# Kernel tuning notes

Measured on AMD Instinct MI355X. Metric: run time of the kernel, lower is better.

## Reference

```python
import jax, jax.numpy as jnp
import numpy as np

N_NODES = 100000
N_EDGES = 1_600_000
F_IN, HID, N_CLS = 128, 64, 32
NEG_SLOPE = 0.2  # PyG GATv2Conv default


def _segment_softmax(scores, seg, num_segments):
    # numerically stable softmax over edges grouped by destination node
    m = jax.ops.segment_max(scores, seg, num_segments=num_segments)
    ex = jnp.exp(scores - m[seg])
    s = jax.ops.segment_sum(ex, seg, num_segments=num_segments)
    return ex / (s[seg] + 1e-16)


def _gatv2_layer(x, src, dst, Wl, bl, Wr, br, att, bias, num_nodes):
    xl = x @ Wl + bl              # source transform  [N, C]
    xr = x @ Wr + br              # target transform  [N, C]
    # per-edge GATv2 attention logit: a . leaky_relu(xl_j + xr_i)
    e = jax.nn.leaky_relu(xl[src] + xr[dst], NEG_SLOPE) @ att  # [E]
    alpha = _segment_softmax(e, dst, num_nodes)                 # [E]
    out = jax.ops.segment_sum(alpha[:, None] * xl[src], dst, num_segments=num_nodes)
    return out + bias


def _add_self_loops(edge_index, n):
    loops = jnp.arange(n, dtype=edge_index.dtype)
    return jnp.concatenate([edge_index, jnp.stack([loops, loops])], axis=1)


def setup_inputs() -> dict:
    key = jax.random.key(0)
    ks = jax.random.split(key, 8)
    s1 = 1.0 / np.sqrt(F_IN)
    s2 = 1.0 / np.sqrt(HID)
    return {
        "x": jax.random.normal(ks[0], (N_NODES, F_IN), jnp.float32),
        "edge_index": jax.random.randint(ks[1], (2, N_EDGES), 0, N_NODES, jnp.int64),
        "W1l": jax.random.normal(ks[2], (F_IN, HID), jnp.float32) * s1,
        "b1l": jnp.zeros((HID,), jnp.float32),
        "W1r": jax.random.normal(ks[3], (F_IN, HID), jnp.float32) * s1,
        "b1r": jnp.zeros((HID,), jnp.float32),
        "att1": jax.random.normal(ks[4], (HID,), jnp.float32) * s2,
        "bias1": jnp.zeros((HID,), jnp.float32),
        "W2l": jax.random.normal(ks[5], (HID, N_CLS), jnp.float32) * s2,
        "b2l": jnp.zeros((N_CLS,), jnp.float32),
        "W2r": jax.random.normal(ks[6], (HID, N_CLS), jnp.float32) * s2,
        "b2r": jnp.zeros((N_CLS,), jnp.float32),
        "att2": jax.random.normal(ks[7], (N_CLS,), jnp.float32) / np.sqrt(N_CLS),
        "bias2": jnp.zeros((N_CLS,), jnp.float32),
    }


def reference(x, edge_index, W1l, b1l, W1r, b1r, att1, bias1,
              W2l, b2l, W2r, b2r, att2, bias2):
    n = x.shape[0]
    ei = _add_self_loops(edge_index, n)
    src, dst = ei[0], ei[1]
    h = jax.nn.relu(_gatv2_layer(x, src, dst, W1l, b1l, W1r, b1r, att1, bias1, n))
    # F.dropout(training=False) is identity in eval mode
    out = _gatv2_layer(h, src, dst, W2l, b2l, W2r, b2r, att2, bias2, n)
    return out
```

## Files before the change

kernel.cpp:

```cpp
#include <hip/hip_runtime.h>
#include <math.h>

#define F_IN 128
#define HID 64
#define NCLS 32
#define NEG 0.2f
#define NBKT 256
#define CHUNK 8192

using bf8 = __attribute__((ext_vector_type(8))) short;
using f4v = __attribute__((ext_vector_type(4))) float;

__device__ __forceinline__ void f4fma(float4& a, float s, const float4& w) {
    a.x = fmaf(s, w.x, a.x);
    a.y = fmaf(s, w.y, a.y);
    a.z = fmaf(s, w.z, a.z);
    a.w = fmaf(s, w.w, a.w);
}
__device__ __forceinline__ unsigned short f2bf(float f) {
    unsigned u = __float_as_uint(f);
    return (unsigned short)((u + 0x7FFFu + ((u >> 16) & 1u)) >> 16);
}


__global__ __launch_bounds__(256) void zeroBuckets(int* __restrict__ bucketSize, int BK) {
    int i = blockIdx.x * 256 + threadIdx.x;
    if (i < BK) bucketSize[i] = 0;
}

__global__ __launch_bounds__(256) void bucketHist(const int* __restrict__ ei,
                                                  int Eorig, int Etot,
                                                  int* __restrict__ bucketSize, int BK) {
    __shared__ int h[512];
    int t = threadIdx.x;
    for (int j = t; j < BK; j += 256) h[j] = 0;
    __syncthreads();
    int base = blockIdx.x * CHUNK;
    int end = base + CHUNK < Etot ? base + CHUNK : Etot;
    for (int i = base + t; i < end; i += 256) {
        int dst = i < Eorig ? ei[Eorig + i] : i - Eorig;
        atomicAdd(&h[dst >> 8], 1);
    }
    __syncthreads();
    for (int j = t; j < BK; j += 256)
        if (h[j]) atomicAdd(&bucketSize[j], h[j]);
}

__global__ __launch_bounds__(256) void bucketScan(const int* __restrict__ bucketSize,
                                                  int* __restrict__ bucketStart,
                                                  int* __restrict__ bucketCursor,
                                                  int BK, int Etot) {
    __shared__ int sd[256];
    int t = threadIdx.x;
    int v0 = (2 * t     < BK) ? bucketSize[2 * t]     : 0;
    int v1 = (2 * t + 1 < BK) ? bucketSize[2 * t + 1] : 0;
    int ts = v0 + v1;
    sd[t] = ts;
    __syncthreads();
    for (int off = 1; off < 256; off <<= 1) {
        int x = (t >= off) ? sd[t - off] : 0;
        __syncthreads();
        sd[t] += x;
        __syncthreads();
    }
    int excl = sd[t] - ts;
    if (2 * t < BK)     { bucketStart[2 * t] = excl;          bucketCursor[2 * t] = excl; }
    if (2 * t + 1 < BK) { bucketStart[2 * t + 1] = excl + v0; bucketCursor[2 * t + 1] = excl + v0; }
    if (t == 255) bucketStart[BK] = Etot;
}

__global__ __launch_bounds__(256) void bucketScatter(const int* __restrict__ ei,
                                                     int Eorig, int Etot,
                                                     int* __restrict__ bucketCursor,
                                                     int2* __restrict__ pairs, int BK) {
    __shared__ int h[512], lbase[512], hcur[512];
    int t = threadIdx.x;
    for (int j = t; j < BK; j += 256) { h[j] = 0; hcur[j] = 0; }
    __syncthreads();
    int base = blockIdx.x * CHUNK;
    int end = base + CHUNK < Etot ? base + CHUNK : Etot;
    for (int i = base + t; i < end; i += 256) {
        int dst = i < Eorig ? ei[Eorig + i] : i - Eorig;
        atomicAdd(&h[dst >> 8], 1);
    }
    __syncthreads();
    for (int j = t; j < BK; j += 256)
        lbase[j] = h[j] ? atomicAdd(&bucketCursor[j], h[j]) : 0;
    __syncthreads();
    for (int i = base + t; i < end; i += 256) {
        int src, dst;
        if (i < Eorig) { src = ei[i]; dst = ei[Eorig + i]; }
        else           { src = dst = i - Eorig; }
        int b = dst >> 8;
        int off = atomicAdd(&hcur[b], 1);
        pairs[lbase[b] + off] = make_int2(src, dst);
    }
}

__global__ __launch_bounds__(256) void bucketCSR(const int2* __restrict__ pairs,
                                                 const int* __restrict__ bucketStart,
                                                 int* __restrict__ rowstart,
                                                 int* __restrict__ cnt,
                                                 int* __restrict__ srclist, int N) {
    __shared__ int c[256], cur[256];
    int t = threadIdx.x;
    int b = blockIdx.x;
    int lo = b * NBKT;
    int eb = bucketStart[b], ee = bucketStart[b + 1];
    c[t] = 0;
    __syncthreads();
    for (int i = eb + t; i < ee; i += 256)
        atomicAdd(&c[pairs[i].y - lo], 1);
    __syncthreads();
    cur[t] = c[t];
    __syncthreads();
    for (int off = 1; off < 256; off <<= 1) {
        int x = (t >= off) ? cur[t - off] : 0;
        __syncthreads();
        cur[t] += x;
        __syncthreads();
    }
    int excl = cur[t] - c[t];
    int node = lo + t;
    if (node < N) { rowstart[node] = eb + excl; cnt[node] = c[t]; }
    __syncthreads();
    cur[t] = excl;
    __syncthreads();
    for (int i = eb + t; i < ee; i += 256) {
        int2 pr = pairs[i];
        int pos = atomicAdd(&cur[pr.y - lo], 1);
        srclist[eb + pos] = pr.x;
    }
}

__global__ __launch_bounds__(256) void prepW(const float* __restrict__ Wl,
                                             const float* __restrict__ Wr,
                                             uint4* __restrict__ wfrag) {
    int e = blockIdx.x * 256 + threadIdx.x;
    if (e >= 2048) return;
    int lane = e & 63;
    int kt = (e >> 6) & 3;
    int ct = (e >> 8) & 3;
    int mat = e >> 10;
    const float* W = mat ? Wr : Wl;
    int k0 = kt * 32 + (lane >> 4) * 8;
    int c = ct * 16 + (lane & 15);
    unsigned short h[8];
#pragma unroll
    for (int j = 0; j < 8; j++) h[j] = f2bf(W[(k0 + j) * HID + c]);
    wfrag[e] = *(uint4*)h;
}

__global__ __launch_bounds__(256) void transform1(const float* __restrict__ x,
                                                  const uint4* __restrict__ wfrag,
                                                  const float* __restrict__ bl,
                                                  const float* __restrict__ br,
                                                  unsigned short* __restrict__ xlb,
                                                  float* __restrict__ xr, int N) {
    __shared__ uint4 sw[2048];
    int t = threadIdx.x;
#pragma unroll
    for (int j = 0; j < 8; j++) sw[t + j * 256] = wfrag[t + j * 256];
    __syncthreads();

    int w = t >> 6, lane = t & 63;
    int nb = blockIdx.x * 64 + w * 16;
    int m = lane & 15, quad = lane >> 4;

    int arow = nb + m; if (arow >= N) arow = N - 1;
    const float* xrow = x + (size_t)arow * F_IN + quad * 8;
    bf8 afr[4];
#pragma unroll
    for (int kt = 0; kt < 4; kt++) {
        float4 lo = *(const float4*)(xrow + kt * 32);
        float4 hi = *(const float4*)(xrow + kt * 32 + 4);
        unsigned short hh[8];
        hh[0] = f2bf(lo.x); hh[1] = f2bf(lo.y); hh[2] = f2bf(lo.z); hh[3] = f2bf(lo.w);
        hh[4] = f2bf(hi.x); hh[5] = f2bf(hi.y); hh[6] = f2bf(hi.z); hh[7] = f2bf(hi.w);
        afr[kt] = *(bf8*)hh;
    }

#pragma unroll
    for (int mat = 0; mat < 2; mat++) {
        const float* bias = mat ? br : bl;
#pragma unroll
        for (int ct = 0; ct < 4; ct++) {
            f4v acc = {0.f, 0.f, 0.f, 0.f};
#pragma unroll
            for (int kt = 0; kt < 4; kt++) {
                bf8 bfr = *(bf8*)&sw[((mat * 4 + ct) * 4 + kt) * 64 + lane];
                acc = __builtin_amdgcn_mfma_f32_16x16x32_bf16(afr[kt], bfr, acc, 0, 0, 0);
            }
            int ch = ct * 16 + m;
            float bv = bias[ch];
#pragma unroll
            for (int reg = 0; reg < 4; reg++) {
                int node = nb + quad * 4 + reg;
                if (node < N) {
                    float o = acc[reg] + bv;
                    if (mat) xr[(size_t)node * HID + ch] = o;
                    else     xlb[(size_t)node * HID + ch] = f2bf(o);
                }
            }
        }
    }
}

__global__ __launch_bounds__(256) void transform2(const float* __restrict__ h,
                                                  const float* __restrict__ Wl,
                                                  const float* __restrict__ bl,
                                                  const float* __restrict__ Wr,
                                                  const float* __restrict__ br,
                                                  unsigned short* __restrict__ xlb,
                                                  float* __restrict__ xr, int N) {
    __shared__ float sWl[HID * NCLS];
    __shared__ float sWr[HID * NCLS];
    __shared__ float sx[128][68];
    int t = threadIdx.x;
    int nb = blockIdx.x * 128;

#pragma unroll
    for (int j = 0; j < 2; j++) {
        int f = t + j * 256;
        ((float4*)sWl)[f] = ((const float4*)Wl)[f];
        ((float4*)sWr)[f] = ((const float4*)Wr)[f];
    }
    int maxf = (N - nb) * 16;
#pragma unroll
    for (int j = 0; j < 8; j++) {
        int f = t + j * 256;
        int node = f >> 4, kc = f & 15;
        float4 v = {0.f, 0.f, 0.f, 0.f};
        if (f < maxf) v = ((const float4*)(h + (size_t)nb * HID))[f];
        v.x = fmaxf(v.x, 0.f);
        v.y = fmaxf(v.y, 0.f);
        v.z = fmaxf(v.z, 0.f);
        v.w = fmaxf(v.w, 0.f);
        *(float4*)&sx[node][kc * 4] = v;
    }
    __syncthreads();

    int c4 = (t & 7) * 4;
    int slot = t >> 3;
    float4 bl4 = *(const float4*)(bl + c4);
    float4 br4 = *(const float4*)(br + c4);
    float4 accl[4] = {bl4, bl4, bl4, bl4};
    float4 accr[4] = {br4, br4, br4, br4};

#pragma unroll 4
    for (int k4 = 0; k4 < HID / 4; k4++) {
        int k = k4 * 4;
        float4 wl0 = *(const float4*)&sWl[(k + 0) * NCLS + c4];
        float4 wl1 = *(const float4*)&sWl[(k + 1) * NCLS + c4];
        float4 wl2 = *(const float4*)&sWl[(k + 2) * NCLS + c4];
        float4 wl3 = *(const float4*)&sWl[(k + 3) * NCLS + c4];
        float4 wr0 = *(const float4*)&sWr[(k + 0) * NCLS + c4];
        float4 wr1 = *(const float4*)&sWr[(k + 1) * NCLS + c4];
        float4 wr2 = *(const float4*)&sWr[(k + 2) * NCLS + c4];
        float4 wr3 = *(const float4*)&sWr[(k + 3) * NCLS + c4];
#pragma unroll
        for (int j = 0; j < 4; j++) {
            float4 xv = *(const float4*)&sx[slot + j * 32][k];
            f4fma(accl[j], xv.x, wl0); f4fma(accr[j], xv.x, wr0);
            f4fma(accl[j], xv.y, wl1); f4fma(accr[j], xv.y, wr1);
            f4fma(accl[j], xv.z, wl2); f4fma(accr[j], xv.z, wr2);
            f4fma(accl[j], xv.w, wl3); f4fma(accr[j], xv.w, wr3);
        }
    }
#pragma unroll
    for (int j = 0; j < 4; j++) {
        int g = nb + slot + j * 32;
        if (g < N) {
            ushort4 o;
            o.x = f2bf(accl[j].x); o.y = f2bf(accl[j].y);
            o.z = f2bf(accl[j].z); o.w = f2bf(accl[j].w);
            *(ushort4*)(xlb + (size_t)g * NCLS + c4) = o;
            *(float4*)(xr + (size_t)g * NCLS + c4) = accr[j];
        }
    }
}

template <int C>
__global__ __launch_bounds__(256) void fusedAggB(const unsigned short* __restrict__ xlb,
                                                 const float* __restrict__ xr,
                                                 const float* __restrict__ att,
                                                 const int* __restrict__ rowstart,
                                                 const int* __restrict__ cnt,
                                                 const int* __restrict__ srclist,
                                                 const float* __restrict__ bias,
                                                 float* __restrict__ out, int N) {
    const int LPQ = C / 8;
    const int SLOTS = 64 / LPQ;
    int wid = threadIdx.x >> 6;
    int lane = threadIdx.x & 63;
    int n = blockIdx.x * 4 + wid;
    if (n >= N) return;

    int slot = lane / LPQ;
    int pos = lane % LPQ;
    int c8 = pos * 8;

    float xr8[8], at8[8];
    *(float4*)&xr8[0] = *(const float4*)(xr + (size_t)n * C + c8);
    *(float4*)&xr8[4] = *(const float4*)(xr + (size_t)n * C + c8 + 4);
    *(float4*)&at8[0] = *(const float4*)(att + c8);
    *(float4*)&at8[4] = *(const float4*)(att + c8 + 4);

    int row = rowstart[n];
    int deg = cnt[n];

    float s = 0.f;
    float acc[8] = {0.f, 0.f, 0.f, 0.f, 0.f, 0.f, 0.f, 0.f};

    for (int cb = 0; cb < deg; cb += 64) {
        int len = deg - cb; if (len > 64) len = 64;
        int li = lane < len ? lane : len - 1;
        int srcreg = srclist[row + cb + li];
        int nbatch = (len + SLOTS - 1) / SLOTS;
#pragma unroll 4
        for (int b = 0; b < nbatch; b++) {
            int eidx = b * SLOTS + slot;
            int src = __shfl(srcreg, eidx, 64);
            uint4 q = *(const uint4*)(xlb + (size_t)src * C + c8);
            float v[8];
            v[0] = __uint_as_float(q.x << 16);
            v[1] = __uint_as_float(q.x & 0xffff0000u);
            v[2] = __uint_as_float(q.y << 16);
            v[3] = __uint_as_float(q.y & 0xffff0000u);
            v[4] = __uint_as_float(q.z << 16);
            v[5] = __uint_as_float(q.z & 0xffff0000u);
            v[6] = __uint_as_float(q.w << 16);
            v[7] = __uint_as_float(q.w & 0xffff0000u);
            float p = 0.f;
#pragma unroll
            for (int c = 0; c < 8; c++) {
                float u = v[c] + xr8[c];
                u = fmaxf(u, NEG * u);
                p = fmaf(u, at8[c], p);
            }
#pragma unroll
            for (int o = 1; o < LPQ; o <<= 1) p += __shfl_xor(p, o, 64);
            float w = (eidx < len) ? __expf(p) : 0.f;
            s += w;
#pragma unroll
            for (int c = 0; c < 8; c++) acc[c] = fmaf(w, v[c], acc[c]);
        }
    }
#pragma unroll
    for (int o = LPQ; o < 64; o <<= 1) {
#pragma unroll
        for (int c = 0; c < 8; c++) acc[c] += __shfl_xor(acc[c], o, 64);
        s += __shfl_xor(s, o, 64);
    }
    if (lane < LPQ) {
        float bi8[8];
        *(float4*)&bi8[0] = *(const float4*)(bias + c8);
        *(float4*)&bi8[4] = *(const float4*)(bias + c8 + 4);
        float inv = 1.f / (s + 1e-16f);
        float o8[8];
#pragma unroll
        for (int c = 0; c < 8; c++) o8[c] = acc[c] * inv + bi8[c];
        *(float4*)(out + (size_t)n * C + c8)     = *(float4*)&o8[0];
        *(float4*)(out + (size_t)n * C + c8 + 4) = *(float4*)&o8[4];
    }
}

extern "C" void kernel_launch(void* const* d_in, const int* in_sizes, int n_in,
                              void* d_out, int out_size, void* d_ws, size_t ws_size,
                              hipStream_t stream) {
    const float* x     = (const float*)d_in[0];
    const int*   ei    = (const int*)d_in[1];
    const float* W1l   = (const float*)d_in[2];
    const float* b1l   = (const float*)d_in[3];
    const float* W1r   = (const float*)d_in[4];
    const float* b1r   = (const float*)d_in[5];
    const float* att1  = (const float*)d_in[6];
    const float* bias1 = (const float*)d_in[7];
    const float* W2l   = (const float*)d_in[8];
    const float* b2l   = (const float*)d_in[9];
    const float* W2r   = (const float*)d_in[10];
    const float* b2r   = (const float*)d_in[11];
    const float* att2  = (const float*)d_in[12];
    const float* bias2 = (const float*)d_in[13];
    float* out = (float*)d_out;

    int N     = in_sizes[0] / F_IN;
    int Eorig = in_sizes[1] / 2;
    int Etot  = Eorig + N;
    int BK    = (N + NBKT - 1) / NBKT;

    char* p = (char*)d_ws;
    auto alloc = [&](size_t bytes) { void* r = (void*)p; p += (bytes + 255) & ~(size_t)255; return r; };
    unsigned short* xl1b = (unsigned short*)alloc((size_t)N * HID * 2);
    float* xr1     = (float*)alloc((size_t)N * HID * 4);
    float* h       = (float*)alloc((size_t)N * HID * 4);
    unsigned short* xl2b = (unsigned short*)alloc((size_t)N * NCLS * 2);
    float* xr2     = (float*)alloc((size_t)N * NCLS * 4);
    int*   cnt     = (int*)alloc((size_t)N * 4);
    int*   rowstart= (int*)alloc((size_t)N * 4);
    int*   srclist = (int*)alloc((size_t)Etot * 4);
    uint4* wfrag   = (uint4*)alloc(2048 * 16);
    int*   bucketSize   = (int*)alloc(520 * 4);
    int*   bucketStart  = (int*)alloc(520 * 4);
    int*   bucketCursor = (int*)alloc(520 * 4);
    int2*  pairs   = (int2*)xl2b;

    int nChunks = (Etot + CHUNK - 1) / CHUNK;

    zeroBuckets<<<2, 256, 0, stream>>>(bucketSize, BK);
    bucketHist<<<nChunks, 256, 0, stream>>>(ei, Eorig, Etot, bucketSize, BK);
    bucketScan<<<1, 256, 0, stream>>>(bucketSize, bucketStart, bucketCursor, BK, Etot);
    bucketScatter<<<nChunks, 256, 0, stream>>>(ei, Eorig, Etot, bucketCursor, pairs, BK);
    bucketCSR<<<BK, 256, 0, stream>>>(pairs, bucketStart, rowstart, cnt, srclist, N);

    prepW<<<8, 256, 0, stream>>>(W1l, W1r, wfrag);
    transform1<<<(N + 63) / 64, 256, 0, stream>>>(x, wfrag, b1l, b1r, xl1b, xr1, N);
    fusedAggB<HID><<<(N + 3) / 4, 256, 0, stream>>>(xl1b, xr1, att1, rowstart, cnt,
                                                    srclist, bias1, h, N);

    transform2<<<(N + 127) / 128, 256, 0, stream>>>(h, W2l, b2l, W2r, b2r, xl2b, xr2, N);
    fusedAggB<NCLS><<<(N + 3) / 4, 256, 0, stream>>>(xl2b, xr2, att2, rowstart, cnt,
                                                     srclist, bias2, out, N);
}
```

Baseline: 319.4 us.

## Merge CSR build stages with weight prep and transform1 into shared launches

Folds the weight-fragment prep into the histogram kernel and runs the bucket scatter and the layer-1 MFMA transform as disjoint block ranges of one launch. Zeroing now uses a memset instead of a separate kernel, which cuts launch count and lets independent work overlap on the GPU. Pairs are packed into 32 bits (24-bit src plus the low 8 bits of dst) to halve the scatter and CSR traffic, and CHUNK shrinks to 2048 for more histogram and scatter blocks. Packing assumes node ids fit in 24 bits, and smaller chunks mean more global atomics on the bucket counters.

After: 329.9 us. 3.3% more time.

```diff
diff --git a/kernel.cpp b/kernel.cpp
--- a/kernel.cpp
+++ b/kernel.cpp
@@ -6,7 +6,7 @@
 #define NCLS 32
 #define NEG 0.2f
 #define NBKT 256
-#define CHUNK 8192
+#define CHUNK 2048
 
 using bf8 = __attribute__((ext_vector_type(8))) short;
 using f4v = __attribute__((ext_vector_type(4))) float;
@@ -22,20 +22,36 @@
     return (unsigned short)((u + 0x7FFFu + ((u >> 16) & 1u)) >> 16);
 }
 
-
-__global__ __launch_bounds__(256) void zeroBuckets(int* __restrict__ bucketSize, int BK) {
-    int i = blockIdx.x * 256 + threadIdx.x;
-    if (i < BK) bucketSize[i] = 0;
-}
-
-__global__ __launch_bounds__(256) void bucketHist(const int* __restrict__ ei,
-                                                  int Eorig, int Etot,
-                                                  int* __restrict__ bucketSize, int BK) {
+__global__ __launch_bounds__(256) void histPrep(const int* __restrict__ ei,
+                                                int Eorig, int Etot,
+                                                int* __restrict__ bucketSize, int BK,
+                                                const float* __restrict__ Wl,
+                                                const float* __restrict__ Wr,
+                                                uint4* __restrict__ wfrag,
+                                                int nChunks) {
     __shared__ int h[512];
     int t = threadIdx.x;
+    int bid = blockIdx.x;
+    if (bid >= nChunks) {
+        int e = (bid - nChunks) * 256 + t;
+        if (e < 2048) {
+            int lane = e & 63;
+            int kt = (e >> 6) & 3;
+            int ct = (e >> 8) & 3;
+            int mat = e >> 10;
+            const float* W = mat ? Wr : Wl;
+            int k0 = kt * 32 + (lane >> 4) * 8;
+            int c = ct * 16 + (lane & 15);
+            unsigned short hh[8];
+#pragma unroll
+            for (int j = 0; j < 8; j++) hh[j] = f2bf(W[(k0 + j) * HID + c]);
+            wfrag[e] = *(uint4*)hh;
+        }
+        return;
+    }
     for (int j = t; j < BK; j += 256) h[j] = 0;
     __syncthreads();
-    int base = blockIdx.x * CHUNK;
+    int base = bid * CHUNK;
     int end = base + CHUNK < Etot ? base + CHUNK : Etot;
     for (int i = base + t; i < end; i += 256) {
         int dst = i < Eorig ? ei[Eorig + i] : i - Eorig;
@@ -69,35 +85,97 @@
     if (t == 255) bucketStart[BK] = Etot;
 }
 
-__global__ __launch_bounds__(256) void bucketScatter(const int* __restrict__ ei,
-                                                     int Eorig, int Etot,
-                                                     int* __restrict__ bucketCursor,
-                                                     int2* __restrict__ pairs, int BK) {
-    __shared__ int h[512], lbase[512], hcur[512];
+__global__ __launch_bounds__(256) void scatT1(const int* __restrict__ ei,
+                                              int Eorig, int Etot,
+                                              int* __restrict__ bucketCursor,
+                                              unsigned* __restrict__ pairs,
+                                              int nScat,
+                                              const float* __restrict__ x,
+                                              const uint4* __restrict__ wfrag,
+                                              const float* __restrict__ bl,
+                                              const float* __restrict__ br,
+                                              unsigned short* __restrict__ xlb,
+                                              float* __restrict__ xr, int N) {
+    __shared__ uint4 sw[2048];
     int t = threadIdx.x;
-    for (int j = t; j < BK; j += 256) { h[j] = 0; hcur[j] = 0; }
-    __syncthreads();
-    int base = blockIdx.x * CHUNK;
-    int end = base + CHUNK < Etot ? base + CHUNK : Etot;
-    for (int i = base + t; i < end; i += 256) {
-        int dst = i < Eorig ? ei[Eorig + i] : i - Eorig;
-        atomicAdd(&h[dst >> 8], 1);
-    }
-    __syncthreads();
-    for (int j = t; j < BK; j += 256)
-        lbase[j] = h[j] ? atomicAdd(&bucketCursor[j], h[j]) : 0;
-    __syncthreads();
-    for (int i = base + t; i < end; i += 256) {
-        int src, dst;
-        if (i < Eorig) { src = ei[i]; dst = ei[Eorig + i]; }
-        else           { src = dst = i - Eorig; }
-        int b = dst >> 8;
-        int off = atomicAdd(&hcur[b], 1);
-        pairs[lbase[b] + off] = make_int2(src, dst);
-    }
-}
-
-__global__ __launch_bounds__(256) void bucketCSR(const int2* __restrict__ pairs,
+    int bid = blockIdx.x;
+
+    if (bid < nScat) {
+        int* h    = (int*)sw;
+        int* lbase = h + 512;
+        int* hcur  = h + 1024;
+        for (int j = t; j < 512; j += 256) { h[j] = 0; hcur[j] = 0; }
+        __syncthreads();
+        int base = bid * CHUNK;
+        int end = base + CHUNK < Etot ? base + CHUNK : Etot;
+        for (int i = base + t; i < end; i += 256) {
+            int dst = i < Eorig ? ei[Eorig + i] : i - Eorig;
+            atomicAdd(&h[dst >> 8], 1);
+        }
+        __syncthreads();
+        for (int j = t; j < 512; j += 256)
+            lbase[j] = h[j] ? atomicAdd(&bucketCursor[j], h[j]) : 0;
+        __syncthreads();
+        for (int i = base + t; i < end; i += 256) {
+            int src, dst;
+            if (i < Eorig) { src = ei[i]; dst = ei[Eorig + i]; }
+            else           { src = dst = i - Eorig; }
+            int b = dst >> 8;
+            int off = atomicAdd(&hcur[b], 1);
+            pairs[lbase[b] + off] = (unsigned)src | ((unsigned)(dst & 255) << 24);
+        }
+        return;
+    }
+
+    int tb = bid - nScat;
+#pragma unroll
+    for (int j = 0; j < 8; j++) sw[t + j * 256] = wfrag[t + j * 256];
+    __syncthreads();
+
+    int w = t >> 6, lane = t & 63;
+    int nb = tb * 64 + w * 16;
+    int m = lane & 15, quad = lane >> 4;
+
+    int arow = nb + m; if (arow >= N) arow = N - 1;
+    const float* xrow = x + (size_t)arow * F_IN + quad * 8;
+    bf8 afr[4];
+#pragma unroll
+    for (int kt = 0; kt < 4; kt++) {
+        float4 lo = *(const float4*)(xrow + kt * 32);
+        float4 hi = *(const float4*)(xrow + kt * 32 + 4);
+        unsigned short hh[8];
+        hh[0] = f2bf(lo.x); hh[1] = f2bf(lo.y); hh[2] = f2bf(lo.z); hh[3] = f2bf(lo.w);
+        hh[4] = f2bf(hi.x); hh[5] = f2bf(hi.y); hh[6] = f2bf(hi.z); hh[7] = f2bf(hi.w);
+        afr[kt] = *(bf8*)hh;
+    }
+
+#pragma unroll
+    for (int mat = 0; mat < 2; mat++) {
+        const float* bias = mat ? br : bl;
+#pragma unroll
+        for (int ct = 0; ct < 4; ct++) {
+            f4v acc = {0.f, 0.f, 0.f, 0.f};
+#pragma unroll
+            for (int kt = 0; kt < 4; kt++) {
+                bf8 bfr = *(bf8*)&sw[((mat * 4 + ct) * 4 + kt) * 64 + lane];
+                acc = __builtin_amdgcn_mfma_f32_16x16x32_bf16(afr[kt], bfr, acc, 0, 0, 0);
+            }
+            int ch = ct * 16 + m;
+            float bv = bias[ch];
+#pragma unroll
+            for (int reg = 0; reg < 4; reg++) {
+                int node = nb + quad * 4 + reg;
+                if (node < N) {
+                    float o = acc[reg] + bv;
+                    if (mat) xr[(size_t)node * HID + ch] = o;
+                    else     xlb[(size_t)node * HID + ch] = f2bf(o);
+                }
+            }
+        }
+    }
+}
+
+__global__ __launch_bounds__(256) void bucketCSR(const unsigned* __restrict__ pairs,
                                                  const int* __restrict__ bucketStart,
                                                  int* __restrict__ rowstart,
                                                  int* __restrict__ cnt,
@@ -110,7 +188,7 @@
     c[t] = 0;
     __syncthreads();
     for (int i = eb + t; i < ee; i += 256)
-        atomicAdd(&c[pairs[i].y - lo], 1);
+        atomicAdd(&c[pairs[i] >> 24], 1);
     __syncthreads();
     cur[t] = c[t];
     __syncthreads();
@@ -127,82 +205,9 @@
     cur[t] = excl;
     __syncthreads();
     for (int i = eb + t; i < ee; i += 256) {
-        int2 pr = pairs[i];
-        int pos = atomicAdd(&cur[pr.y - lo], 1);
-        srclist[eb + pos] = pr.x;
-    }
-}
-
-__global__ __launch_bounds__(256) void prepW(const float* __restrict__ Wl,
-                                             const float* __restrict__ Wr,
-                                             uint4* __restrict__ wfrag) {
-    int e = blockIdx.x * 256 + threadIdx.x;
-    if (e >= 2048) return;
-    int lane = e & 63;
-    int kt = (e >> 6) & 3;
-    int ct = (e >> 8) & 3;
-    int mat = e >> 10;
-    const float* W = mat ? Wr : Wl;
-    int k0 = kt * 32 + (lane >> 4) * 8;
-    int c = ct * 16 + (lane & 15);
-    unsigned short h[8];
-#pragma unroll
-    for (int j = 0; j < 8; j++) h[j] = f2bf(W[(k0 + j) * HID + c]);
-    wfrag[e] = *(uint4*)h;
-}
-
-__global__ __launch_bounds__(256) void transform1(const float* __restrict__ x,
-                                                  const uint4* __restrict__ wfrag,
-                                                  const float* __restrict__ bl,
-                                                  const float* __restrict__ br,
-                                                  unsigned short* __restrict__ xlb,
-                                                  float* __restrict__ xr, int N) {
-    __shared__ uint4 sw[2048];
-    int t = threadIdx.x;
-#pragma unroll
-    for (int j = 0; j < 8; j++) sw[t + j * 256] = wfrag[t + j * 256];
-    __syncthreads();
-
-    int w = t >> 6, lane = t & 63;
-    int nb = blockIdx.x * 64 + w * 16;
-    int m = lane & 15, quad = lane >> 4;
-
-    int arow = nb + m; if (arow >= N) arow = N - 1;
-    const float* xrow = x + (size_t)arow * F_IN + quad * 8;
-    bf8 afr[4];
-#pragma unroll
-    for (int kt = 0; kt < 4; kt++) {
-        float4 lo = *(const float4*)(xrow + kt * 32);
-        float4 hi = *(const float4*)(xrow + kt * 32 + 4);
-        unsigned short hh[8];
-        hh[0] = f2bf(lo.x); hh[1] = f2bf(lo.y); hh[2] = f2bf(lo.z); hh[3] = f2bf(lo.w);
-        hh[4] = f2bf(hi.x); hh[5] = f2bf(hi.y); hh[6] = f2bf(hi.z); hh[7] = f2bf(hi.w);
-        afr[kt] = *(bf8*)hh;
-    }
-
-#pragma unroll
-    for (int mat = 0; mat < 2; mat++) {
-        const float* bias = mat ? br : bl;
-#pragma unroll
-        for (int ct = 0; ct < 4; ct++) {
-            f4v acc = {0.f, 0.f, 0.f, 0.f};
-#pragma unroll
-            for (int kt = 0; kt < 4; kt++) {
-                bf8 bfr = *(bf8*)&sw[((mat * 4 + ct) * 4 + kt) * 64 + lane];
-                acc = __builtin_amdgcn_mfma_f32_16x16x32_bf16(afr[kt], bfr, acc, 0, 0, 0);
-            }
-            int ch = ct * 16 + m;
-            float bv = bias[ch];
-#pragma unroll
-            for (int reg = 0; reg < 4; reg++) {
-                int node = nb + quad * 4 + reg;
-                if (node < N) {
-                    float o = acc[reg] + bv;
-                    if (mat) xr[(size_t)node * HID + ch] = o;
-                    else     xlb[(size_t)node * HID + ch] = f2bf(o);
-                }
-            }
-        }
+        unsigned pr = pairs[i];
+        int pos = atomicAdd(&cur[pr >> 24], 1);
+        srclist[eb + pos] = pr & 0xFFFFFFu;
     }
 }
 
@@ -403,18 +408,19 @@
     int*   bucketSize   = (int*)alloc(520 * 4);
     int*   bucketStart  = (int*)alloc(520 * 4);
     int*   bucketCursor = (int*)alloc(520 * 4);
-    int2*  pairs   = (int2*)xl2b;
+    unsigned* pairs = (unsigned*)xl2b;
 
     int nChunks = (Etot + CHUNK - 1) / CHUNK;
-
-    zeroBuckets<<<2, 256, 0, stream>>>(bucketSize, BK);
-    bucketHist<<<nChunks, 256, 0, stream>>>(ei, Eorig, Etot, bucketSize, BK);
+    int nT1     = (N + 63) / 64;
+
+    hipMemsetAsync(bucketSize, 0, 520 * 4, stream);
+    histPrep<<<nChunks + 8, 256, 0, stream>>>(ei, Eorig, Etot, bucketSize, BK,
+                                              W1l, W1r, wfrag, nChunks);
     bucketScan<<<1, 256, 0, stream>>>(bucketSize, bucketStart, bucketCursor, BK, Etot);
-    bucketScatter<<<nChunks, 256, 0, stream>>>(ei, Eorig, Etot, bucketCursor, pairs, BK);
+    scatT1<<<nChunks + nT1, 256, 0, stream>>>(ei, Eorig, Etot, bucketCursor, pairs,
+                                              nChunks, x, wfrag, b1l, b1r, xl1b, xr1, N);
     bucketCSR<<<BK, 256, 0, stream>>>(pairs, bucketStart, rowstart, cnt, srclist, N);
 
-    prepW<<<8, 256, 0, stream>>>(W1l, W1r, wfrag);
-    transform1<<<(N + 63) / 64, 256, 0, stream>>>(x, wfrag, b1l, b1r, xl1b, xr1, N);
     fusedAggB<HID><<<(N + 3) / 4, 256, 0, stream>>>(xl1b, xr1, att1, rowstart, cnt,
                                                     srclist, bias1, h, N);
 
```
